# Kernel optimization log

Hardware: AMD Instinct MI355X
Metric: run time of the kernel (lower is better)

## Reference

```python
import jax, jax.numpy as jnp
import numpy as np

PATCH_SIZE = [3, 5, 7]
PATCH_SEQ = [5, 7]
SEQ_SIZE = 6
WIN = 210
D_MODEL = 256
B, M = 8, 55
EPS = 1e-5


def _loo(p):
    # leave-one-out index matrix, row i = all indices except i -> (p, p-1)
    return np.array([[k for k in range(p) if k != i] for i in range(p)], dtype=np.int32)


def _mlp(x, W1, b1, W2, b2):
    # torch MLP: fc2(relu(fc1(x))), Linear weights are (out, in)
    h = jax.nn.relu(x @ W1.T + b1)
    return h @ W2.T + b2


def _forward(x, sP, nP, ssP, nsP):
    Bn, L, Mn = x.shape
    # RevIN 'norm' with fresh affine (weight=1, bias=0): identity affine; stats detached
    mean = jax.lax.stop_gradient(jnp.mean(x, axis=1, keepdims=True))
    std = jax.lax.stop_gradient(jnp.sqrt(jnp.var(x, axis=1, keepdims=True) + EPS))
    xn = (x - mean) / std
    xt = jnp.transpose(xn, (0, 2, 1)).reshape(Bn * Mn, L)  # (BM, L)
    sm, pm, ssr, psr = [], [], [], []
    for j, p in enumerate(PATCH_SIZE):
        n = L // p
        x3 = xt.reshape(Bn * Mn, p, n)  # l = r*n + k
        # size branch: leave-one-out over the p axis, blocks ordered i*n + k
        feat = jnp.transpose(x3[:, _loo(p), :], (0, 1, 3, 2)).reshape(Bn * Mn, L, p - 1)
        y = _mlp(feat, *sP[j])[..., 0]  # (BM, L)
        sm.append(jnp.transpose(y.reshape(Bn, Mn, L), (0, 2, 1)))
        # num branch: leave-one-out over the n axis of row l%p, leaving out column l//p
        g = _mlp(x3[:, :, _loo(n)], *nP[j])[..., 0]  # (BM, p, n)
        # torch cats over l (axis 0) then reshapes (B, M, L): flat order is (l, b, m)
        prior = jnp.transpose(g, (2, 1, 0)).reshape(Bn, Mn, L)  # faithful scrambled reshape
        pm.append(jnp.transpose(prior, (0, 2, 1)))
    s = SEQ_SIZE
    for j, p in enumerate(PATCH_SEQ):
        n = L // (p * s)
        x4 = xt.reshape(Bn * Mn, p, n, s)  # l = (r*n + k)*s + t
        # size_seq branch: leave-one-out over p, feature = (p-1)*s per (i, k) position
        feat = jnp.transpose(x4[:, _loo(p)], (0, 1, 3, 2, 4)).reshape(Bn * Mn, p * n, (p - 1) * s)
        y = _mlp(feat, *ssP[j])  # (BM, p*n, s)
        ssr.append(jnp.transpose(y.reshape(Bn, Mn, L), (0, 2, 1)))
        # num_seq branch: leave-one-out over n, cat order i*p + r
        featn = jnp.transpose(x4[:, :, _loo(n), :], (0, 2, 1, 3, 4)).reshape(Bn * Mn, n * p, (n - 1) * s)
        g = _mlp(featn, *nsP[j])  # (BM, n*p, s)
        d0 = PATCH_SEQ[0]  # original code hardcodes patch_seq[0] here
        h = jnp.transpose(g.reshape(Bn, Mn, (n * p) // d0, d0, s), (0, 1, 3, 2, 4)).reshape(Bn, Mn, L)
        psr.append(jnp.transpose(h, (0, 2, 1)))
    # original returns 4 lists of (B, L, M); stack all 10 for a single output
    return jnp.stack(sm + pm + ssr + psr, axis=0)


def setup_inputs() -> dict:
    key = jax.random.key(0)
    keys = iter(jax.random.split(key, 128))
    d = {"x": jax.random.normal(next(keys), (B, WIN, M), dtype=jnp.float32)}

    def lin(name, out_d, in_d):
        d[name + "W"] = jax.random.normal(next(keys), (out_d, in_d), dtype=jnp.float32) / np.float32(np.sqrt(in_d))
        d[name + "b"] = jax.random.normal(next(keys), (out_d,), dtype=jnp.float32) * np.float32(0.01)

    for j, p in enumerate(PATCH_SIZE):
        lin(f"s1_{j}", D_MODEL, p - 1)
        lin(f"s2_{j}", 1, D_MODEL)
        lin(f"n1_{j}", D_MODEL, WIN // p - 1)
        lin(f"n2_{j}", 1, D_MODEL)
    for j, p in enumerate(PATCH_SEQ):
        lin(f"ss1_{j}", D_MODEL, (p - 1) * SEQ_SIZE)
        lin(f"ss2_{j}", SEQ_SIZE, D_MODEL)
        lin(f"ns1_{j}", D_MODEL, WIN // p - SEQ_SIZE)
        lin(f"ns2_{j}", SEQ_SIZE, D_MODEL)
    return d


def reference(x, s1_0W, s1_0b, s2_0W, s2_0b, n1_0W, n1_0b, n2_0W, n2_0b,
              s1_1W, s1_1b, s2_1W, s2_1b, n1_1W, n1_1b, n2_1W, n2_1b,
              s1_2W, s1_2b, s2_2W, s2_2b, n1_2W, n1_2b, n2_2W, n2_2b,
              ss1_0W, ss1_0b, ss2_0W, ss2_0b, ns1_0W, ns1_0b, ns2_0W, ns2_0b,
              ss1_1W, ss1_1b, ss2_1W, ss2_1b, ns1_1W, ns1_1b, ns2_1W, ns2_1b):
    sP = [(s1_0W, s1_0b, s2_0W, s2_0b), (s1_1W, s1_1b, s2_1W, s2_1b), (s1_2W, s1_2b, s2_2W, s2_2b)]
    nP = [(n1_0W, n1_0b, n2_0W, n2_0b), (n1_1W, n1_1b, n2_1W, n2_1b), (n1_2W, n1_2b, n2_2W, n2_2b)]
    ssP = [(ss1_0W, ss1_0b, ss2_0W, ss2_0b), (ss1_1W, ss1_1b, ss2_1W, ss2_1b)]
    nsP = [(ns1_0W, ns1_0b, ns2_0W, ns2_0b), (ns1_1W, ns1_1b, ns2_1W, ns2_1b)]
    return _forward(x, sP, nP, ssP, nsP)
```

## Files before the change

### kernel.cpp

```cpp
#include <hip/hip_runtime.h>

#define LL  210
#define MM  55
#define NBM 440
#define DM  256
#define MLT 11550
#define BLM 92400

#define XTG_OFF  0
#define W1T_OFF  92400
#define REC_OFF  158704

__device__ __forceinline__ float wave_sum(float v) {
#pragma unroll
    for (int off = 32; off > 0; off >>= 1) v += __shfl_xor(v, off, 64);
    return v;
}

__device__ __forceinline__ void fma4(float4& a, const float4 w, const float s) {
    a.x += w.x * s; a.y += w.y * s; a.z += w.z * s; a.w += w.w * s;
}
__device__ __forceinline__ void fms4(float4& a, const float4 w, const float s) {
    a.x -= w.x * s; a.y -= w.y * s; a.z -= w.z * s; a.w -= w.w * s;
}

__device__ __forceinline__ float bfly8(const float y[8], const int lane) {
    float z[4];
#pragma unroll
    for (int i = 0; i < 4; ++i) {
        float snd = (lane & 1) ? y[2*i] : y[2*i+1];
        float rcv = __shfl_xor(snd, 1, 64);
        z[i] = ((lane & 1) ? y[2*i+1] : y[2*i]) + rcv;
    }
    float u[2];
#pragma unroll
    for (int i = 0; i < 2; ++i) {
        float snd = (lane & 2) ? z[2*i] : z[2*i+1];
        float rcv = __shfl_xor(snd, 2, 64);
        u[i] = ((lane & 2) ? z[2*i+1] : z[2*i]) + rcv;
    }
    {
        float snd = (lane & 4) ? u[0] : u[1];
        float rcv = __shfl_xor(snd, 4, 64);
        float w = ((lane & 4) ? u[1] : u[0]) + rcv;
        w += __shfl_xor(w, 8, 64);
        w += __shfl_xor(w, 16, 64);
        w += __shfl_xor(w, 32, 64);
        return w;
    }
}

__global__ __launch_bounds__(256) void knorm_trans(
        const float* __restrict__ x,
        const float* __restrict__ nw0, const float* __restrict__ nw1, const float* __restrict__ nw2,
        const float* __restrict__ ssw0, const float* __restrict__ ssw1,
        const float* __restrict__ nsw0, const float* __restrict__ nsw1,
        const float* __restrict__ s1W0, const float* __restrict__ s1b0, const float* __restrict__ s2W0,
        const float* __restrict__ s1W1, const float* __restrict__ s1b1, const float* __restrict__ s2W1,
        const float* __restrict__ s1W2, const float* __restrict__ s1b2, const float* __restrict__ s2W2,
        float* __restrict__ xtg, float* __restrict__ w1t, float* __restrict__ recs) {
    __shared__ float red[4];
    const int t = threadIdx.x;
    const int blk = blockIdx.x;
    if (blk < NBM) {
        const int bm = blk, b = bm / MM, m = bm % MM;
        const int wid = t >> 6, lane = t & 63;
        float v = (t < LL) ? x[b * MLT + t * MM + m] : 0.f;
        float sv = wave_sum(v);
        if (lane == 0) red[wid] = sv;
        __syncthreads();
        float mean = (red[0] + red[1] + red[2] + red[3]) * (1.f / 210.f);
        __syncthreads();
        float dv = (t < LL) ? v - mean : 0.f;
        float sq = wave_sum(dv * dv);
        if (lane == 0) red[wid] = sq;
        __syncthreads();
        float var = (red[0] + red[1] + red[2] + red[3]) * (1.f / 210.f);
        float inv = rsqrtf(var + 1e-5f);
        if (t < LL) xtg[(bm >> 3) * 1680 + t * 8 + (bm & 7)] = dv * inv;
    } else if (blk < NBM + 259) {
        const int e = (blk - NBM) * 256 + t;
        const int cg = e >> 8, d = e & 255;
        const float* src; int ind, c;
        if (cg < 69)       { src = nw0;  ind = 69; c = cg; }
        else if (cg < 110) { src = nw1;  ind = 41; c = cg - 69; }
        else if (cg < 139) { src = nw2;  ind = 29; c = cg - 110; }
        else if (cg < 163) { src = ssw0; ind = 24; c = cg - 139; }
        else if (cg < 199) { src = ssw1; ind = 36; c = cg - 163; }
        else if (cg < 235) { src = nsw0; ind = 36; c = cg - 199; }
        else               { src = nsw1; ind = 24; c = cg - 235; }
        w1t[cg * DM + d] = src[d * ind + c];
    } else {
        const int e = (blk - NBM - 259) * 256 + t;
        float v;
        if (e < 1024) {
            int d = e >> 2, c = e & 3;
            v = (c < 2) ? s1W0[d * 2 + c] : (c == 2 ? s1b0[d] : s2W0[d]);
        } else if (e < 3072) {
            int rel = e - 1024, d = rel >> 3, c = rel & 7;
            v = (c < 4) ? s1W1[d * 4 + c] : (c == 4 ? s1b1[d] : (c == 5 ? s2W1[d] : 0.f));
        } else {
            int rel = e - 3072, d = rel >> 3, c = rel & 7;
            v = (c < 6) ? s1W2[d * 6 + c] : (c == 6 ? s1b2[d] : s2W2[d]);
        }
        recs[e] = v;
    }
}

template <int IND>
__device__ __forceinline__ void ksize_body(const float* __restrict__ xtg,
        const float* __restrict__ rec, const float* __restrict__ b2,
        int bm, int j, float* __restrict__ out) {
    constexpr int N = LL / (IND + 1);
    const int t = threadIdx.x;
    if (t >= LL) return;
    const float* xs = xtg + (bm >> 3) * 1680 + (bm & 7);
    const int i = t / N, k = t - i * N;
    float f[IND];
#pragma unroll
    for (int idx = 0; idx < IND; ++idx) {
        int row = idx + (idx >= i);
        f[idx] = xs[(row * N + k) * 8];
    }
    float y = b2[0];
    const float4* r4 = (const float4*)rec;
    if constexpr (IND == 2) {
#pragma unroll 8
        for (int d = 0; d < DM; ++d) {
            const float4 rv = r4[d];
            y += fmaxf(rv.x * f[0] + rv.y * f[1] + rv.z, 0.f) * rv.w;
        }
    } else if constexpr (IND == 4) {
#pragma unroll 4
        for (int d = 0; d < DM; ++d) {
            const float4 a = r4[2 * d], b = r4[2 * d + 1];
            y += fmaxf(a.x*f[0] + a.y*f[1] + a.z*f[2] + a.w*f[3] + b.x, 0.f) * b.y;
        }
    } else {
#pragma unroll 4
        for (int d = 0; d < DM; ++d) {
            const float4 a = r4[2 * d], b = r4[2 * d + 1];
            y += fmaxf(a.x*f[0] + a.y*f[1] + a.z*f[2] + a.w*f[3] + b.x*f[4] + b.y*f[5] + b.z, 0.f) * b.w;
        }
    }
    const int b_ = bm / MM, m = bm - b_ * MM;
    out[j * BLM + b_ * MLT + t * MM + m] = y;
}

__global__ __launch_bounds__(256) void ksize_all(const float* __restrict__ xtg,
        const float* __restrict__ recs,
        const float* __restrict__ b2_0, const float* __restrict__ b2_1, const float* __restrict__ b2_2,
        float* __restrict__ out) {
    const int blk = blockIdx.x;
    if (blk < NBM)          ksize_body<2>(xtg, recs,        b2_0, blk,           0, out);
    else if (blk < 2 * NBM) ksize_body<4>(xtg, recs + 1024, b2_1, blk - NBM,     1, out);
    else                    ksize_body<6>(xtg, recs + 3072, b2_2, blk - 2 * NBM, 2, out);
}

template <int P, int N>
__device__ __forceinline__ void knum_body(const float* __restrict__ xtg,
        const float* __restrict__ wt, const float* __restrict__ b1,
        const float* __restrict__ W2, const float* __restrict__ b2,
        int grp, int r, int j, float* __restrict__ out) {
    const int t = threadIdx.x, wid = t >> 6, lane = t & 63;
    const int g0 = wid * 2;
    const float* xb = xtg + grp * 1680 + r * N * 8 + g0;
    const float4 b1v = *(const float4*)&b1[lane * 4];
    const float4 w2v = *(const float4*)&W2[lane * 4];
    const float b2v = b2[0];
    const float* wl = wt + lane * 4;
    float4 A0 = b1v, A1 = b1v;
    float4 B0 = make_float4(0.f,0.f,0.f,0.f), B1 = B0;
#pragma unroll 2
    for (int q = 1; q < N; ++q) {
        const float4 w = *(const float4*)(wl + (q - 1) * DM);
        const float2 xv = *(const float2*)(xb + q * 8);
        fma4(B0, w, xv.x); fma4(B1, w, xv.y);
    }
    constexpr int NFULL = N / 8, TAIL = N - NFULL * 8;
    for (int c = 0; c <= NFULL; ++c) {
        float y0[8], y1[8];
        const bool full = (c < NFULL);
#pragma unroll
        for (int i = 0; i < 8; ++i) {
            const int k = c * 8 + i;
            if (full || i < TAIL) {
                float hx = fmaxf(A0.x + B0.x, 0.f), hy = fmaxf(A0.y + B0.y, 0.f);
                float hz = fmaxf(A0.z + B0.z, 0.f), hw = fmaxf(A0.w + B0.w, 0.f);
                y0[i] = hx * w2v.x + hy * w2v.y + hz * w2v.z + hw * w2v.w;
                hx = fmaxf(A1.x + B1.x, 0.f); hy = fmaxf(A1.y + B1.y, 0.f);
                hz = fmaxf(A1.z + B1.z, 0.f); hw = fmaxf(A1.w + B1.w, 0.f);
                y1[i] = hx * w2v.x + hy * w2v.y + hz * w2v.z + hw * w2v.w;
                if (full || i < TAIL - 1) {
                    const float4 w = *(const float4*)(wl + k * DM);
                    const float2 xk  = *(const float2*)(xb + k * 8);
                    const float2 xk1 = *(const float2*)(xb + k * 8 + 8);
                    fma4(A0, w, xk.x);  fma4(A1, w, xk.y);
                    fms4(B0, w, xk1.x); fms4(B1, w, xk1.y);
                }
            } else { y0[i] = 0.f; y1[i] = 0.f; }
        }
        const float v0 = bfly8(y0, lane), v1 = bfly8(y1, lane);
        if (lane < 16) {
            const int k = c * 8 + (lane & 7);
            if (k < N) {
                const int bm = grp * 8 + g0 + (lane >> 3);
                const float val = ((lane < 8) ? v0 : v1) + b2v;
                const int fi = (k * P + r) * NBM + bm;
                const int ob = fi / MLT, rem = fi - ob * MLT;
                const int om = rem / LL, ol = rem - om * LL;
                out[(3 + j) * BLM + ob * MLT + ol * MM + om] = val;
            }
        }
    }
}

__global__ __launch_bounds__(256) void knum_all(const float* __restrict__ xtg,
        const float* __restrict__ w1t,
        const float* __restrict__ b1_0, const float* __restrict__ W2_0, const float* __restrict__ b2_0,
        const float* __restrict__ b1_1, const float* __restrict__ W2_1, const float* __restrict__ b2_1,
        const float* __restrict__ b1_2, const float* __restrict__ W2_2, const float* __restrict__ b2_2,
        float* __restrict__ out) {
    const int blk = blockIdx.x;
    if (blk < 165) {
        int rel = blk;       knum_body<3, 70>(xtg, w1t,            b1_0, W2_0, b2_0, rel / 3, rel % 3, 0, out);
    } else if (blk < 440) {
        int rel = blk - 165; knum_body<5, 42>(xtg, w1t + 69 * DM,  b1_1, W2_1, b2_1, rel / 5, rel % 5, 1, out);
    } else {
        int rel = blk - 440; knum_body<7, 30>(xtg, w1t + 110 * DM, b1_2, W2_2, b2_2, rel / 7, rel % 7, 2, out);
    }
}

template <int ISNUM, int P, int N>
__device__ __forceinline__ void kseq_body(const float* __restrict__ xtg,
        const float* __restrict__ w1tb, const float* __restrict__ b1,
        const float* __restrict__ W2, const float* __restrict__ b2,
        int grp, int slab, float* __restrict__ out) {
    constexpr int NROWS = ISNUM ? (N - 1) : (P - 1);
    const int t = threadIdx.x, wid = t >> 6, lane = t & 63;
    const float4 b1v = *(const float4*)&b1[lane * 4];
    const float* xg = xtg + grp * 1680;
    float b2r[6];
#pragma unroll
    for (int tt = 0; tt < 6; ++tt) b2r[tt] = b2[tt];
    const int bm = grp * 8 + (lane & 7);
    const int b_ = bm / MM, m = bm - b_ * MM;
    for (int q = wid; q < 35; q += 4) {
        int pivot, fix;
        if (ISNUM) { pivot = q / P; fix = q - pivot * P; }
        else       { pivot = q / N; fix = q - pivot * N; }
        float4 acc[8];
#pragma unroll
        for (int g = 0; g < 8; ++g) acc[g] = b1v;
        const float* wl = w1tb + lane * 4;
        for (int idx = 0; idx < NROWS; ++idx) {
            const int row = idx + (idx >= pivot);
            const int pos0 = ISNUM ? (fix * N + row) * 6 : (row * N + fix) * 6;
            const float* xp = xg + pos0 * 8;
#pragma unroll
            for (int tt = 0; tt < 6; ++tt) {
                const float4 xa = *(const float4*)(xp + tt * 8);
                const float4 xc = *(const float4*)(xp + tt * 8 + 4);
                const float4 w  = *(const float4*)wl; wl += DM;
                fma4(acc[0], w, xa.x); fma4(acc[1], w, xa.y);
                fma4(acc[2], w, xa.z); fma4(acc[3], w, xa.w);
                fma4(acc[4], w, xc.x); fma4(acc[5], w, xc.y);
                fma4(acc[6], w, xc.z); fma4(acc[7], w, xc.w);
            }
        }
#pragma unroll
        for (int g = 0; g < 8; ++g) {
            acc[g].x = fmaxf(acc[g].x, 0.f); acc[g].y = fmaxf(acc[g].y, 0.f);
            acc[g].z = fmaxf(acc[g].z, 0.f); acc[g].w = fmaxf(acc[g].w, 0.f);
        }
        const int c2 = q / 5, dd = q - c2 * 5;
#pragma unroll
        for (int h = 0; h < 2; ++h) {
            float yv0[8], yv1[8], yv2[8];
#pragma unroll
            for (int tt2 = 0; tt2 < 3; ++tt2) {
                const int tt = h * 3 + tt2;
                const float4 w2v = *(const float4*)&W2[tt * DM + lane * 4];
                float* yv = (tt2 == 0) ? yv0 : ((tt2 == 1) ? yv1 : yv2);
#pragma unroll
                for (int g = 0; g < 8; ++g)
                    yv[g] = acc[g].x * w2v.x + acc[g].y * w2v.y + acc[g].z * w2v.z + acc[g].w * w2v.w;
            }
            const float r0 = bfly8(yv0, lane);
            const float r1 = bfly8(yv1, lane);
            const float r2 = bfly8(yv2, lane);
            if (lane < 8) {
#pragma unroll
                for (int tt2 = 0; tt2 < 3; ++tt2) {
                    const int tt = h * 3 + tt2;
                    const int l = ISNUM ? (dd * 42 + c2 * 6 + tt) : (q * 6 + tt);
                    const float rv = (tt2 == 0) ? r0 : ((tt2 == 1) ? r1 : r2);
                    out[slab + b_ * MLT + l * MM + m] = rv + b2r[tt];
                }
            }
        }
    }
}

__global__ __launch_bounds__(256) void kseq_all(const float* __restrict__ xtg,
        const float* __restrict__ w1t,
        const float* __restrict__ ss1b0, const float* __restrict__ ss2W0, const float* __restrict__ ss2b0,
        const float* __restrict__ ss1b1, const float* __restrict__ ss2W1, const float* __restrict__ ss2b1,
        const float* __restrict__ ns1b0, const float* __restrict__ ns2W0, const float* __restrict__ ns2b0,
        const float* __restrict__ ns1b1, const float* __restrict__ ns2W1, const float* __restrict__ ns2b1,
        float* __restrict__ out) {
    const int blk = blockIdx.x;
    const int tc = blk / 55, grp = blk - tc * 55;
    if (tc == 0)      kseq_body<0, 5, 7>(xtg, w1t + 139 * DM, ss1b0, ss2W0, ss2b0, grp, 6 * BLM, out);
    else if (tc == 1) kseq_body<0, 7, 5>(xtg, w1t + 163 * DM, ss1b1, ss2W1, ss2b1, grp, 7 * BLM, out);
    else if (tc == 2) kseq_body<1, 5, 7>(xtg, w1t + 199 * DM, ns1b0, ns2W0, ns2b0, grp, 8 * BLM, out);
    else              kseq_body<1, 7, 5>(xtg, w1t + 235 * DM, ns1b1, ns2W1, ns2b1, grp, 9 * BLM, out);
}

extern "C" void kernel_launch(void* const* d_in, const int* in_sizes, int n_in,
                              void* d_out, int out_size, void* d_ws, size_t ws_size,
                              hipStream_t stream) {
    (void)in_sizes; (void)n_in; (void)out_size; (void)ws_size;
    const float* x = (const float*)d_in[0];
    const float *s1W[3], *s1b[3], *s2W[3], *s2b[3], *n1W[3], *n1b[3], *n2W[3], *n2b[3];
    for (int j = 0; j < 3; ++j) {
        int base = 1 + j * 8;
        s1W[j] = (const float*)d_in[base + 0]; s1b[j] = (const float*)d_in[base + 1];
        s2W[j] = (const float*)d_in[base + 2]; s2b[j] = (const float*)d_in[base + 3];
        n1W[j] = (const float*)d_in[base + 4]; n1b[j] = (const float*)d_in[base + 5];
        n2W[j] = (const float*)d_in[base + 6]; n2b[j] = (const float*)d_in[base + 7];
    }
    const float *ss1W[2], *ss1b[2], *ss2W[2], *ss2b[2], *ns1W[2], *ns1b[2], *ns2W[2], *ns2b[2];
    for (int j = 0; j < 2; ++j) {
        int base = 25 + j * 8;
        ss1W[j] = (const float*)d_in[base + 0]; ss1b[j] = (const float*)d_in[base + 1];
        ss2W[j] = (const float*)d_in[base + 2]; ss2b[j] = (const float*)d_in[base + 3];
        ns1W[j] = (const float*)d_in[base + 4]; ns1b[j] = (const float*)d_in[base + 5];
        ns2W[j] = (const float*)d_in[base + 6]; ns2b[j] = (const float*)d_in[base + 7];
    }
    float* out  = (float*)d_out;
    float* xtg  = (float*)d_ws + XTG_OFF;
    float* w1t  = (float*)d_ws + W1T_OFF;
    float* recs = (float*)d_ws + REC_OFF;

    knorm_trans<<<719, 256, 0, stream>>>(x,
        n1W[0], n1W[1], n1W[2],
        ss1W[0], ss1W[1], ns1W[0], ns1W[1],
        s1W[0], s1b[0], s2W[0],
        s1W[1], s1b[1], s2W[1],
        s1W[2], s1b[2], s2W[2],
        xtg, w1t, recs);
    ksize_all<<<1320, 256, 0, stream>>>(xtg, recs, s2b[0], s2b[1], s2b[2], out);
    knum_all<<<825, 256, 0, stream>>>(xtg, w1t,
        n1b[0], n2W[0], n2b[0],
        n1b[1], n2W[1], n2b[1],
        n1b[2], n2W[2], n2b[2], out);
    kseq_all<<<220, 256, 0, stream>>>(xtg, w1t,
        ss1b[0], ss2W[0], ss2b[0],
        ss1b[1], ss2W[1], ss2b[1],
        ns1b[0], ns2W[0], ns2b[0],
        ns1b[1], ns2W[1], ns2b[1], out);
}
```

Before: 246.6 us.

## Fuse size, num and seq kernels into one launch and split seq work

Merges the three compute kernels (size, num, seq branches) into a single launch with block-index dispatch. This removes two launch boundaries and lets the branches run concurrently on the GPU. The seq branch is also split four ways over its q loop, giving 880 blocks instead of 220 so that small phase has more parallelism. In addition, the size-branch reduction uses two independent accumulators for more ILP, and the RevIN stats are computed in a single pass using E[x^2]-mean^2, which drops a barrier but is slightly less numerically robust.

```diff
diff --git a/kernel.cpp b/kernel.cpp
--- a/kernel.cpp
+++ b/kernel.cpp
@@ -59,25 +59,22 @@
         const float* __restrict__ s1W1, const float* __restrict__ s1b1, const float* __restrict__ s2W1,
         const float* __restrict__ s1W2, const float* __restrict__ s1b2, const float* __restrict__ s2W2,
         float* __restrict__ xtg, float* __restrict__ w1t, float* __restrict__ recs) {
-    __shared__ float red[4];
+    __shared__ float red[8];
     const int t = threadIdx.x;
     const int blk = blockIdx.x;
     if (blk < NBM) {
         const int bm = blk, b = bm / MM, m = bm % MM;
         const int wid = t >> 6, lane = t & 63;
         float v = (t < LL) ? x[b * MLT + t * MM + m] : 0.f;
-        float sv = wave_sum(v);
-        if (lane == 0) red[wid] = sv;
+        float s1 = wave_sum(v);
+        float s2 = wave_sum(v * v);
+        if (lane == 0) { red[wid] = s1; red[4 + wid] = s2; }
         __syncthreads();
         float mean = (red[0] + red[1] + red[2] + red[3]) * (1.f / 210.f);
-        __syncthreads();
-        float dv = (t < LL) ? v - mean : 0.f;
-        float sq = wave_sum(dv * dv);
-        if (lane == 0) red[wid] = sq;
-        __syncthreads();
-        float var = (red[0] + red[1] + red[2] + red[3]) * (1.f / 210.f);
+        float msq  = (red[4] + red[5] + red[6] + red[7]) * (1.f / 210.f);
+        float var = msq - mean * mean;
         float inv = rsqrtf(var + 1e-5f);
-        if (t < LL) xtg[(bm >> 3) * 1680 + t * 8 + (bm & 7)] = dv * inv;
+        if (t < LL) xtg[(bm >> 3) * 1680 + t * 8 + (bm & 7)] = (v - mean) * inv;
     } else if (blk < NBM + 259) {
         const int e = (blk - NBM) * 256 + t;
         const int cg = e >> 8, d = e & 255;
@@ -122,39 +119,34 @@
         int row = idx + (idx >= i);
         f[idx] = xs[(row * N + k) * 8];
     }
-    float y = b2[0];
+    float y0 = b2[0], y1 = 0.f;
     const float4* r4 = (const float4*)rec;
     if constexpr (IND == 2) {
 #pragma unroll 8
-        for (int d = 0; d < DM; ++d) {
-            const float4 rv = r4[d];
-            y += fmaxf(rv.x * f[0] + rv.y * f[1] + rv.z, 0.f) * rv.w;
+        for (int d = 0; d < DM; d += 2) {
+            const float4 a = r4[d], b = r4[d + 1];
+            y0 += fmaxf(a.x * f[0] + a.y * f[1] + a.z, 0.f) * a.w;
+            y1 += fmaxf(b.x * f[0] + b.y * f[1] + b.z, 0.f) * b.w;
         }
     } else if constexpr (IND == 4) {
-#pragma unroll 4
-        for (int d = 0; d < DM; ++d) {
-            const float4 a = r4[2 * d], b = r4[2 * d + 1];
-            y += fmaxf(a.x*f[0] + a.y*f[1] + a.z*f[2] + a.w*f[3] + b.x, 0.f) * b.y;
+#pragma unroll 8
+        for (int d = 0; d < DM; d += 2) {
+            const float4 a = r4[2*d], b = r4[2*d+1];
+            const float4 c = r4[2*d+2], e = r4[2*d+3];
+            y0 += fmaxf(a.x*f[0] + a.y*f[1] + a.z*f[2] + a.w*f[3] + b.x, 0.f) * b.y;
+            y1 += fmaxf(c.x*f[0] + c.y*f[1] + c.z*f[2] + c.w*f[3] + e.x, 0.f) * e.y;
         }
     } else {
-#pragma unroll 4
-        for (int d = 0; d < DM; ++d) {
-            const float4 a = r4[2 * d], b = r4[2 * d + 1];
-            y += fmaxf(a.x*f[0] + a.y*f[1] + a.z*f[2] + a.w*f[3] + b.x*f[4] + b.y*f[5] + b.z, 0.f) * b.w;
+#pragma unroll 8
+        for (int d = 0; d < DM; d += 2) {
+            const float4 a = r4[2*d], b = r4[2*d+1];
+            const float4 c = r4[2*d+2], e = r4[2*d+3];
+            y0 += fmaxf(a.x*f[0] + a.y*f[1] + a.z*f[2] + a.w*f[3] + b.x*f[4] + b.y*f[5] + b.z, 0.f) * b.w;
+            y1 += fmaxf(c.x*f[0] + c.y*f[1] + c.z*f[2] + c.w*f[3] + e.x*f[4] + e.y*f[5] + e.z, 0.f) * e.w;
         }
     }
     const int b_ = bm / MM, m = bm - b_ * MM;
-    out[j * BLM + b_ * MLT + t * MM + m] = y;
-}
-
-__global__ __launch_bounds__(256) void ksize_all(const float* __restrict__ xtg,
-        const float* __restrict__ recs,
-        const float* __restrict__ b2_0, const float* __restrict__ b2_1, const float* __restrict__ b2_2,
-        float* __restrict__ out) {
-    const int blk = blockIdx.x;
-    if (blk < NBM)          ksize_body<2>(xtg, recs,        b2_0, blk,           0, out);
-    else if (blk < 2 * NBM) ksize_body<4>(xtg, recs + 1024, b2_1, blk - NBM,     1, out);
-    else                    ksize_body<6>(xtg, recs + 3072, b2_2, blk - 2 * NBM, 2, out);
+    out[j * BLM + b_ * MLT + t * MM + m] = y0 + y1;
 }
 
 template <int P, int N>
@@ -215,27 +207,11 @@
     }
 }
 
-__global__ __launch_bounds__(256) void knum_all(const float* __restrict__ xtg,
-        const float* __restrict__ w1t,
-        const float* __restrict__ b1_0, const float* __restrict__ W2_0, const float* __restrict__ b2_0,
-        const float* __restrict__ b1_1, const float* __restrict__ W2_1, const float* __restrict__ b2_1,
-        const float* __restrict__ b1_2, const float* __restrict__ W2_2, const float* __restrict__ b2_2,
-        float* __restrict__ out) {
-    const int blk = blockIdx.x;
-    if (blk < 165) {
-        int rel = blk;       knum_body<3, 70>(xtg, w1t,            b1_0, W2_0, b2_0, rel / 3, rel % 3, 0, out);
-    } else if (blk < 440) {
-        int rel = blk - 165; knum_body<5, 42>(xtg, w1t + 69 * DM,  b1_1, W2_1, b2_1, rel / 5, rel % 5, 1, out);
-    } else {
-        int rel = blk - 440; knum_body<7, 30>(xtg, w1t + 110 * DM, b1_2, W2_2, b2_2, rel / 7, rel % 7, 2, out);
-    }
-}
-
 template <int ISNUM, int P, int N>
 __device__ __forceinline__ void kseq_body(const float* __restrict__ xtg,
         const float* __restrict__ w1tb, const float* __restrict__ b1,
         const float* __restrict__ W2, const float* __restrict__ b2,
-        int grp, int slab, float* __restrict__ out) {
+        int grp, int qc, int slab, float* __restrict__ out) {
     constexpr int NROWS = ISNUM ? (N - 1) : (P - 1);
     const int t = threadIdx.x, wid = t >> 6, lane = t & 63;
     const float4 b1v = *(const float4*)&b1[lane * 4];
@@ -245,7 +221,8 @@
     for (int tt = 0; tt < 6; ++tt) b2r[tt] = b2[tt];
     const int bm = grp * 8 + (lane & 7);
     const int b_ = bm / MM, m = bm - b_ * MM;
-    for (int q = wid; q < 35; q += 4) {
+    const int qe = (qc * 9 + 9 < 35) ? (qc * 9 + 9) : 35;
+    for (int q = qc * 9 + wid; q < qe; q += 4) {
         int pivot, fix;
         if (ISNUM) { pivot = q / P; fix = q - pivot * P; }
         else       { pivot = q / N; fix = q - pivot * N; }
@@ -302,19 +279,40 @@
     }
 }
 
-__global__ __launch_bounds__(256) void kseq_all(const float* __restrict__ xtg,
-        const float* __restrict__ w1t,
+__global__ __launch_bounds__(256) void kfused(const float* __restrict__ xtg,
+        const float* __restrict__ w1t, const float* __restrict__ recs,
+        const float* __restrict__ b2s0, const float* __restrict__ b2s1, const float* __restrict__ b2s2,
+        const float* __restrict__ nb1_0, const float* __restrict__ nW2_0, const float* __restrict__ nb2_0,
+        const float* __restrict__ nb1_1, const float* __restrict__ nW2_1, const float* __restrict__ nb2_1,
+        const float* __restrict__ nb1_2, const float* __restrict__ nW2_2, const float* __restrict__ nb2_2,
         const float* __restrict__ ss1b0, const float* __restrict__ ss2W0, const float* __restrict__ ss2b0,
         const float* __restrict__ ss1b1, const float* __restrict__ ss2W1, const float* __restrict__ ss2b1,
         const float* __restrict__ ns1b0, const float* __restrict__ ns2W0, const float* __restrict__ ns2b0,
         const float* __restrict__ ns1b1, const float* __restrict__ ns2W1, const float* __restrict__ ns2b1,
         float* __restrict__ out) {
     const int blk = blockIdx.x;
-    const int tc = blk / 55, grp = blk - tc * 55;
-    if (tc == 0)      kseq_body<0, 5, 7>(xtg, w1t + 139 * DM, ss1b0, ss2W0, ss2b0, grp, 6 * BLM, out);
-    else if (tc == 1) kseq_body<0, 7, 5>(xtg, w1t + 163 * DM, ss1b1, ss2W1, ss2b1, grp, 7 * BLM, out);
-    else if (tc == 2) kseq_body<1, 5, 7>(xtg, w1t + 199 * DM, ns1b0, ns2W0, ns2b0, grp, 8 * BLM, out);
-    else              kseq_body<1, 7, 5>(xtg, w1t + 235 * DM, ns1b1, ns2W1, ns2b1, grp, 9 * BLM, out);
+    if (blk < 1320) {
+        if (blk < NBM)          ksize_body<2>(xtg, recs,        b2s0, blk,           0, out);
+        else if (blk < 2 * NBM) ksize_body<4>(xtg, recs + 1024, b2s1, blk - NBM,     1, out);
+        else                    ksize_body<6>(xtg, recs + 3072, b2s2, blk - 2 * NBM, 2, out);
+    } else if (blk < 2145) {
+        const int bn = blk - 1320;
+        if (bn < 165) {
+            int rel = bn;       knum_body<3, 70>(xtg, w1t,            nb1_0, nW2_0, nb2_0, rel / 3, rel % 3, 0, out);
+        } else if (bn < 440) {
+            int rel = bn - 165; knum_body<5, 42>(xtg, w1t + 69 * DM,  nb1_1, nW2_1, nb2_1, rel / 5, rel % 5, 1, out);
+        } else {
+            int rel = bn - 440; knum_body<7, 30>(xtg, w1t + 110 * DM, nb1_2, nW2_2, nb2_2, rel / 7, rel % 7, 2, out);
+        }
+    } else {
+        const int bs = blk - 2145;
+        const int tc = bs / 220, rem = bs - tc * 220;
+        const int grp = rem >> 2, qc = rem & 3;
+        if (tc == 0)      kseq_body<0, 5, 7>(xtg, w1t + 139 * DM, ss1b0, ss2W0, ss2b0, grp, qc, 6 * BLM, out);
+        else if (tc == 1) kseq_body<0, 7, 5>(xtg, w1t + 163 * DM, ss1b1, ss2W1, ss2b1, grp, qc, 7 * BLM, out);
+        else if (tc == 2) kseq_body<1, 5, 7>(xtg, w1t + 199 * DM, ns1b0, ns2W0, ns2b0, grp, qc, 8 * BLM, out);
+        else              kseq_body<1, 7, 5>(xtg, w1t + 235 * DM, ns1b1, ns2W1, ns2b1, grp, qc, 9 * BLM, out);
+    }
 }
 
 extern "C" void kernel_launch(void* const* d_in, const int* in_sizes, int n_in,
@@ -350,12 +348,11 @@
         s1W[1], s1b[1], s2W[1],
         s1W[2], s1b[2], s2W[2],
         xtg, w1t, recs);
-    ksize_all<<<1320, 256, 0, stream>>>(xtg, recs, s2b[0], s2b[1], s2b[2], out);
-    knum_all<<<825, 256, 0, stream>>>(xtg, w1t,
+    kfused<<<3025, 256, 0, stream>>>(xtg, w1t, recs,
+        s2b[0], s2b[1], s2b[2],
         n1b[0], n2W[0], n2b[0],
         n1b[1], n2W[1], n2b[1],
-        n1b[2], n2W[2], n2b[2], out);
-    kseq_all<<<220, 256, 0, stream>>>(xtg, w1t,
+        n1b[2], n2W[2], n2b[2],
         ss1b[0], ss2W[0], ss2b[0],
         ss1b[1], ss2W[1], ss2b[1],
         ns1b[0], ns2W[0], ns2b[0],
```

New measurement: 222.9 us. -9.6%, faster.
